# Kernel tuning notes

Hardware: AMD Instinct MI355X
Metric: run time of the kernel (lower is better)

Reference implementation:

```python
import jax, jax.numpy as jnp
import numpy as np
from jax import lax

# ---- Loihi neuron constants (params['neuron'], params['simulation']) ----
VTH_MANT = 80
THETA = VTH_MANT * (1 << 6)          # 5120, vThMant scaled by 2^6 weight resolution
I_DECAY = 1024                        # current decay (12-bit fixed point)
V_DECAY = 128                         # voltage decay (12-bit fixed point)
WGT_EXP = 0
WGT_SCALE = 1 << (6 + WGT_EXP)        # 64
TS = 1.0

def _loihi_srm_kernel():
    # integer Loihi simulation of the PSP impulse response (slayerLoihi._calculateLoihiPSP)
    u = 1 << (6 + WGT_EXP)
    v = u
    ker = [v]
    while ker[-1] > 0:
        u = (u * (4096 - I_DECAY)) >> 12
        v = ((v * (4096 - V_DECAY)) >> 12) + u
        ker.append(v)
    return np.asarray(ker, np.float32) / (1 << 6)

SRM_KERNEL = _loihi_srm_kernel()      # ~180 taps, ker[0] = 1

def psp(x):
    # causal FIR over time: y[t] = sum_k x[t-k] * ker[k];  x: [B, C, T]
    B, C, T = x.shape
    K = SRM_KERNEL.shape[0]
    w = jnp.asarray(SRM_KERNEL[::-1].copy()).reshape(1, 1, K).astype(x.dtype)
    y = lax.conv_general_dilated(x.reshape(B * C, 1, T), w, (1,), [(K - 1, 0)],
                                 dimension_numbers=('NCH', 'OIH', 'NCH'))
    return y.reshape(B, C, T)

def _decay(x, d):
    # sign-symmetric arithmetic-shift decay, exactly as the Loihi CUDA kernel
    s = jnp.where(x >= 0, 1, -1).astype(jnp.int32)
    return s * ((s * x * (4096 - d)) >> 12)

def spike_loihi(w):
    # quantized integrate-and-fire; w: [B, C, T] float weighted input
    x = jnp.trunc(w * (WGT_SCALE / TS)).astype(jnp.int32)   # C-style int() truncation
    xt = jnp.moveaxis(x, -1, 0)                             # [T, B, C]
    z = jnp.zeros(x.shape[:-1], jnp.int32)
    def step(carry, xi):
        u, v = carry
        un = _decay(u, I_DECAY) + xi
        vn = _decay(v, V_DECAY) + un
        sp = vn >= THETA
        vn = jnp.where(sp, 0, vn)                           # hard reset on spike
        return (un, vn), (sp, vn)
    _, (s, vrec) = lax.scan(step, (z, z), xt)
    spike = jnp.moveaxis(s, 0, -1).astype(w.dtype) / TS
    voltage = jnp.moveaxis(vrec, 0, -1).astype(w.dtype)
    return spike, voltage

def delay_shift(x):
    # delayShift(x, 1): one-tick axonal delay along time
    return jnp.concatenate([jnp.zeros_like(x[..., :1]), x[..., :-1]], axis=-1)

def setup_inputs():
    key = jax.random.key(0)
    k1, k2, k3 = jax.random.split(key, 3)
    B, CIN, HID, COUT, T = 32, 512, 1024, 256, 512
    spike_input = (jax.random.uniform(k1, (B, CIN, 1, 1, T)) < 0.05).astype(jnp.float32)
    W1 = jax.random.normal(k2, (HID, CIN), jnp.float32) * 0.2
    W2 = jax.random.normal(k3, (COUT, HID), jnp.float32) * 0.2
    return {"spike_input": spike_input, "W1": W1, "W2": W2}

def reference(spike_input, W1, W2):
    x = spike_input[:, :, 0, 0, :]                          # [B, Cin, T]
    s1, _ = spike_loihi(psp(jnp.einsum('oi,bit->bot', W1, x)))
    s1 = delay_shift(s1)
    s2, _ = spike_loihi(psp(jnp.einsum('oh,bht->bot', W2, s1)))
    s2 = delay_shift(s2)
    return s2[:, :, None, None, :]                          # [B, Cout, 1, 1, T]
```

## Files before the change

### kernel.cpp

```cpp
#include <hip/hip_runtime.h>


#pragma clang fp contract(off)

constexpr int kT     = 512;
constexpr int kCIN   = 512;
constexpr int kHID   = 1024;
constexpr int kCOUT  = 256;
constexpr int kB     = 32;
constexpr int kTHETA = 5120;
constexpr int kOT1   = 16;
constexpr int kOT2   = 8;
constexpr int kHP1   = 20;
constexpr int kHP2   = 12;
constexpr int kSBP   = 516;
constexpr int kCURP  = 521;

struct Ker { float v[96]; int n; };
constexpr Ker mk_ker() {
    Ker K{}; int u = 64, v = 64; K.v[0] = 1.0f; int i = 1;
    while (v > 0 && i < 96) {
        u = (u * 3072) >> 12;
        v = ((v * 3968) >> 12) + u;
        K.v[i++] = (float)v / 64.0f;
    }
    K.n = i; return K;
}
constexpr Ker KER = mk_ker();
static_assert(KER.n == 88, "SRM kernel length must be 88");
static_assert(KER.v[87] == 0.0f, "tap 87 must be the exact zero tail tap");
__device__ __constant__ Ker KERC = mk_ker();

__device__ __forceinline__ float2 pkmul(const float2 a, const float b) {
    return make_float2(a.x * b, a.y * b);
}
__device__ __forceinline__ float2 pkadd(const float2 a, const float2 b) {
    return make_float2(a.x + b.x, a.y + b.y);
}

__device__ __forceinline__ int decay_i(int x, int mult) {
    unsigned ax = (x >= 0) ? (unsigned)x : (0u - (unsigned)x);
    unsigned p  = ax * (unsigned)mult;
    int sh = ((int)p) >> 12;
    return (x >= 0) ? sh : (int)(0u - (unsigned)sh);
}

__global__ __launch_bounds__(256) void k0_pack(const float* __restrict__ X,
                                               unsigned* __restrict__ XPW) {
    const int tid = blockIdx.x * 256 + threadIdx.x;
    const int b = tid >> 13, rem = tid & 8191, w = rem >> 9, t = rem & 511;
    const float* xp = X + ((size_t)(b * kCIN + w * 32)) * kT + t;
    unsigned m = 0;
#pragma unroll
    for (int k = 0; k < 32; ++k)
        m |= (xp[(size_t)k * kT] != 0.0f ? 1u : 0u) << k;
    XPW[tid] = m;
}

#define GW16(MW, BASE) { unsigned m_ = (MW); while (m_) { \
    const int bi_ = __ffs(m_) - 1; m_ &= m_ - 1; const int ii_ = (BASE) + bi_; \
    const float4 f0 = *reinterpret_cast<const float4*>(&w0[ii_ * 4]); \
    const float4 f1 = *reinterpret_cast<const float4*>(&w1[ii_ * 4]); \
    const float4 f2 = *reinterpret_cast<const float4*>(&w2[ii_ * 4]); \
    const float4 f3 = *reinterpret_cast<const float4*>(&w3[ii_ * 4]); \
    A0 = pkadd(A0, make_float2(f0.x, f0.y)); A1 = pkadd(A1, make_float2(f0.z, f0.w)); \
    A2 = pkadd(A2, make_float2(f1.x, f1.y)); A3 = pkadd(A3, make_float2(f1.z, f1.w)); \
    A4 = pkadd(A4, make_float2(f2.x, f2.y)); A5 = pkadd(A5, make_float2(f2.z, f2.w)); \
    A6 = pkadd(A6, make_float2(f3.x, f3.y)); A7 = pkadd(A7, make_float2(f3.z, f3.w)); } }

#define ACC16(E0,E1,E2,E3,E4,E5,E6,E7, Q0,Q1,Q2,Q3, KV) \
    E0 = pkadd(E0, pkmul(make_float2(Q0.x, Q0.y), (KV))); \
    E1 = pkadd(E1, pkmul(make_float2(Q0.z, Q0.w), (KV))); \
    E2 = pkadd(E2, pkmul(make_float2(Q1.x, Q1.y), (KV))); \
    E3 = pkadd(E3, pkmul(make_float2(Q1.z, Q1.w), (KV))); \
    E4 = pkadd(E4, pkmul(make_float2(Q2.x, Q2.y), (KV))); \
    E5 = pkadd(E5, pkmul(make_float2(Q2.z, Q2.w), (KV))); \
    E6 = pkadd(E6, pkmul(make_float2(Q3.x, Q3.y), (KV))); \
    E7 = pkadd(E7, pkmul(make_float2(Q3.z, Q3.w), (KV)));

__global__ __launch_bounds__(512, 6) void k1_fused(const unsigned* __restrict__ XPW,
                                                   const float* __restrict__ W,
                                                   unsigned short* __restrict__ SPW) {
    __shared__ __align__(16) unsigned char regn[40960];
    __shared__ unsigned char sbuf[kOT1 * kSBP];

    float* w0    = reinterpret_cast<float*>(regn);
    float* w1    = reinterpret_cast<float*>(regn + 8192);
    float* w2    = reinterpret_cast<float*>(regn + 16384);
    float* w3    = reinterpret_cast<float*>(regn + 24576);
    float* heven = reinterpret_cast<float*>(regn);
    float* hodd  = reinterpret_cast<float*>(regn + 20480);
    int*   cur   = reinterpret_cast<int*>(regn);

    const int t     = threadIdx.x;
    const int b     = blockIdx.x >> 6;
    const int oblk  = blockIdx.x & 63;
    const int obase = oblk * kOT1;

    for (int idx = t; idx < kOT1 * kCIN; idx += 512) {
        const int j = idx >> 9, i = idx & 511;
        float* wq = reinterpret_cast<float*>(regn + (j >> 2) * 8192);
        wq[i * 4 + (j & 3)] = W[(size_t)(obase + j) * kCIN + i];
    }
    __syncthreads();

    const unsigned* xw = XPW + ((size_t)b * 16) * kT + t;
    float2 A0 = make_float2(0.f, 0.f), A1 = A0, A2 = A0, A3 = A0,
           A4 = A0, A5 = A0, A6 = A0, A7 = A0;
    {
        const unsigned m0=xw[0],    m1=xw[512],  m2=xw[1024], m3=xw[1536],
                       m4=xw[2048], m5=xw[2560], m6=xw[3072], m7=xw[3584],
                       m8=xw[4096], m9=xw[4608], mA=xw[5120], mB=xw[5632],
                       mC=xw[6144], mD=xw[6656], mE=xw[7168], mF=xw[7680];
        GW16(m0,0)   GW16(m1,32)  GW16(m2,64)  GW16(m3,96)
        GW16(m4,128) GW16(m5,160) GW16(m6,192) GW16(m7,224)
        GW16(m8,256) GW16(m9,288) GW16(mA,320) GW16(mB,352)
        GW16(mC,384) GW16(mD,416) GW16(mE,448) GW16(mF,480)
    }
    __syncthreads();

    {
        float* hr = ((t & 1) ? hodd : heven) + (size_t)(t >> 1) * kHP1;
        *reinterpret_cast<float4*>(hr + 0)  = make_float4(A0.x, A0.y, A1.x, A1.y);
        *reinterpret_cast<float4*>(hr + 4)  = make_float4(A2.x, A2.y, A3.x, A3.y);
        *reinterpret_cast<float4*>(hr + 8)  = make_float4(A4.x, A4.y, A5.x, A5.y);
        *reinterpret_cast<float4*>(hr + 12) = make_float4(A6.x, A6.y, A7.x, A7.y);
    }
    __syncthreads();

    float2 E0, E1, E2, E3, E4, E5, E6, E7, O0, O1, O2, O3, O4, O5, O6, O7;
    E0=E1=E2=E3=E4=E5=E6=E7=O0=O1=O2=O3=O4=O5=O6=O7 = make_float2(0.f, 0.f);
    const int q = t;
    if (t < 256) {
        for (int j = 0; j < 43; ++j) {
            const int m = q - 43 + j;
            const float t87 = KERC.v[87 - 2 * j];
            const float t86 = KERC.v[86 - 2 * j];
            const float t85 = KERC.v[85 - 2 * j];
            if (m >= 0) {
                const float* he = heven + (size_t)m * kHP1;
                const float* ho = hodd  + (size_t)m * kHP1;
                const float4 a0 = *reinterpret_cast<const float4*>(he + 0);
                const float4 a1 = *reinterpret_cast<const float4*>(he + 4);
                const float4 a2 = *reinterpret_cast<const float4*>(he + 8);
                const float4 a3 = *reinterpret_cast<const float4*>(he + 12);
                const float4 b0 = *reinterpret_cast<const float4*>(ho + 0);
                const float4 b1 = *reinterpret_cast<const float4*>(ho + 4);
                const float4 b2 = *reinterpret_cast<const float4*>(ho + 8);
                const float4 b3 = *reinterpret_cast<const float4*>(ho + 12);
                ACC16(E0,E1,E2,E3,E4,E5,E6,E7, a0,a1,a2,a3, t86)
                ACC16(E0,E1,E2,E3,E4,E5,E6,E7, b0,b1,b2,b3, t85)
                ACC16(O0,O1,O2,O3,O4,O5,O6,O7, a0,a1,a2,a3, t87)
                ACC16(O0,O1,O2,O3,O4,O5,O6,O7, b0,b1,b2,b3, t86)
            }
        }
        {
            const float* he = heven + (size_t)q * kHP1;
            const float* ho = hodd  + (size_t)q * kHP1;
            const float4 a0 = *reinterpret_cast<const float4*>(he + 0);
            const float4 a1 = *reinterpret_cast<const float4*>(he + 4);
            const float4 a2 = *reinterpret_cast<const float4*>(he + 8);
            const float4 a3 = *reinterpret_cast<const float4*>(he + 12);
            const float4 b0 = *reinterpret_cast<const float4*>(ho + 0);
            const float4 b1 = *reinterpret_cast<const float4*>(ho + 4);
            const float4 b2 = *reinterpret_cast<const float4*>(ho + 8);
            const float4 b3 = *reinterpret_cast<const float4*>(ho + 12);
            const float v1 = KERC.v[1];
            ACC16(E0,E1,E2,E3,E4,E5,E6,E7, a0,a1,a2,a3, 1.0f)
            ACC16(O0,O1,O2,O3,O4,O5,O6,O7, a0,a1,a2,a3, v1)
            ACC16(O0,O1,O2,O3,O4,O5,O6,O7, b0,b1,b2,b3, 1.0f)
        }
    }
    __syncthreads();

    if (t < 256) {
#define CST1(CH, EV, OV) \
        cur[(CH) * kCURP + 2 * q]     = (int)((EV) * 64.0f); \
        cur[(CH) * kCURP + 2 * q + 1] = (int)((OV) * 64.0f);
        CST1( 0, E0.x, O0.x) CST1( 1, E0.y, O0.y)
        CST1( 2, E1.x, O1.x) CST1( 3, E1.y, O1.y)
        CST1( 4, E2.x, O2.x) CST1( 5, E2.y, O2.y)
        CST1( 6, E3.x, O3.x) CST1( 7, E3.y, O3.y)
        CST1( 8, E4.x, O4.x) CST1( 9, E4.y, O4.y)
        CST1(10, E5.x, O5.x) CST1(11, E5.y, O5.y)
        CST1(12, E6.x, O6.x) CST1(13, E6.y, O6.y)
        CST1(14, E7.x, O7.x) CST1(15, E7.y, O7.y)
#undef CST1
    }
    __syncthreads();

    if (t < kOT1) {
        const int* cr = cur + t * kCURP;
        int u = 0, v = 0;
        sbuf[t * kSBP + 0] = 0;
        for (int s = 0; s < kT; ++s) {
            const int un = (int)((unsigned)decay_i(u, 3072) + (unsigned)cr[s]);
            int vn = (int)((unsigned)decay_i(v, 3968) + (unsigned)un);
            const int sp_ = (vn >= kTHETA) ? 1 : 0;
            if (sp_) vn = 0;
            u = un; v = vn;
            if (s + 1 < kT) sbuf[t * kSBP + s + 1] = (unsigned char)sp_;
        }
    }
    __syncthreads();

    {
        unsigned lo = 0, hi = 0;
#pragma unroll
        for (int j = 0; j < 8; ++j) {
            lo |= (unsigned)sbuf[j * kSBP + t] << j;
            hi |= (unsigned)sbuf[(8 + j) * kSBP + t] << j;
        }
        SPW[((((size_t)b * 32 + (oblk >> 1)) * kT) + t) * 2 + (oblk & 1)] =
            (unsigned short)(lo | (hi << 8));
    }
}

#define GW8(MW, BASE) { unsigned m_ = (MW); while (m_) { \
    const int bi_ = __ffs(m_) - 1; m_ &= m_ - 1; const int ii_ = (BASE) + bi_; \
    const float4 lo = *reinterpret_cast<const float4*>(&wlo[ii_ * 4]); \
    const float4 hi = *reinterpret_cast<const float4*>(&whi[ii_ * 4]); \
    A0 = pkadd(A0, make_float2(lo.x, lo.y)); A1 = pkadd(A1, make_float2(lo.z, lo.w)); \
    A2 = pkadd(A2, make_float2(hi.x, hi.y)); A3 = pkadd(A3, make_float2(hi.z, hi.w)); } }

#define ACC8(E0,E1,E2,E3, Q0,Q1, KV) \
    E0 = pkadd(E0, pkmul(make_float2(Q0.x, Q0.y), (KV))); \
    E1 = pkadd(E1, pkmul(make_float2(Q0.z, Q0.w), (KV))); \
    E2 = pkadd(E2, pkmul(make_float2(Q1.x, Q1.y), (KV))); \
    E3 = pkadd(E3, pkmul(make_float2(Q1.z, Q1.w), (KV)));

__global__ __launch_bounds__(512, 8) void k2_fused(const unsigned* __restrict__ SPW,
                                                   const float* __restrict__ W,
                                                   float* __restrict__ O) {
    __shared__ __align__(16) unsigned char regn[32768];
    __shared__ unsigned char sbuf[kOT2 * kSBP];

    float* wlo   = reinterpret_cast<float*>(regn);
    float* whi   = reinterpret_cast<float*>(regn + 16384);
    float* heven = reinterpret_cast<float*>(regn);
    float* hodd  = reinterpret_cast<float*>(regn + 12288);
    int*   cur   = reinterpret_cast<int*>(regn);

    const int t     = threadIdx.x;
    const int b     = blockIdx.x >> 5;
    const int obase = (blockIdx.x & 31) * kOT2;

    for (int idx = t; idx < kOT2 * kHID; idx += 512) {
        const int j = idx >> 10, i = idx & 1023;
        const float w = W[(size_t)(obase + j) * kHID + i];
        if (j < 4) wlo[i * 4 + j] = w; else whi[i * 4 + (j - 4)] = w;
    }
    __syncthreads();

    const unsigned* sp = SPW + ((size_t)b * 32) * kT + t;
    float2 A0 = make_float2(0.f, 0.f), A1 = A0, A2 = A0, A3 = A0;
#pragma unroll 4
    for (int g = 0; g < 32; ++g) {
        const unsigned m = sp[(size_t)g * kT];
        GW8(m, g * 32)
    }
    __syncthreads();

    {
        float* hr = ((t & 1) ? hodd : heven) + (size_t)(t >> 1) * kHP2;
        *reinterpret_cast<float4*>(hr + 0) = make_float4(A0.x, A0.y, A1.x, A1.y);
        *reinterpret_cast<float4*>(hr + 4) = make_float4(A2.x, A2.y, A3.x, A3.y);
    }
    __syncthreads();

    float2 E0, E1, E2, E3, O0, O1, O2, O3;
    E0=E1=E2=E3=O0=O1=O2=O3 = make_float2(0.f, 0.f);
    const int q = t;
    if (t < 256) {
        for (int j = 0; j < 43; ++j) {
            const int m = q - 43 + j;
            const float t87 = KERC.v[87 - 2 * j];
            const float t86 = KERC.v[86 - 2 * j];
            const float t85 = KERC.v[85 - 2 * j];
            if (m >= 0) {
                const float* he = heven + (size_t)m * kHP2;
                const float* ho = hodd  + (size_t)m * kHP2;
                const float4 a0 = *reinterpret_cast<const float4*>(he + 0);
                const float4 a1 = *reinterpret_cast<const float4*>(he + 4);
                const float4 b0 = *reinterpret_cast<const float4*>(ho + 0);
                const float4 b1 = *reinterpret_cast<const float4*>(ho + 4);
                ACC8(E0,E1,E2,E3, a0,a1, t86)
                ACC8(E0,E1,E2,E3, b0,b1, t85)
                ACC8(O0,O1,O2,O3, a0,a1, t87)
                ACC8(O0,O1,O2,O3, b0,b1, t86)
            }
        }
        {
            const float* he = heven + (size_t)q * kHP2;
            const float* ho = hodd  + (size_t)q * kHP2;
            const float4 a0 = *reinterpret_cast<const float4*>(he + 0);
            const float4 a1 = *reinterpret_cast<const float4*>(he + 4);
            const float4 b0 = *reinterpret_cast<const float4*>(ho + 0);
            const float4 b1 = *reinterpret_cast<const float4*>(ho + 4);
            const float v1 = KERC.v[1];
            ACC8(E0,E1,E2,E3, a0,a1, 1.0f)
            ACC8(O0,O1,O2,O3, a0,a1, v1)
            ACC8(O0,O1,O2,O3, b0,b1, 1.0f)
        }
    }
    __syncthreads();

    if (t < 256) {
#define CST2(CH, EV, OV) \
        cur[(CH) * kCURP + 2 * q]     = (int)((EV) * 64.0f); \
        cur[(CH) * kCURP + 2 * q + 1] = (int)((OV) * 64.0f);
        CST2(0, E0.x, O0.x) CST2(1, E0.y, O0.y)
        CST2(2, E1.x, O1.x) CST2(3, E1.y, O1.y)
        CST2(4, E2.x, O2.x) CST2(5, E2.y, O2.y)
        CST2(6, E3.x, O3.x) CST2(7, E3.y, O3.y)
#undef CST2
    }
    __syncthreads();

    if (t < kOT2) {
        const int* cr = cur + t * kCURP;
        int u = 0, v = 0;
        sbuf[t * kSBP + 0] = 0;
        for (int s = 0; s < kT; ++s) {
            const int un = (int)((unsigned)decay_i(u, 3072) + (unsigned)cr[s]);
            int vn = (int)((unsigned)decay_i(v, 3968) + (unsigned)un);
            const int sp2 = (vn >= kTHETA) ? 1 : 0;
            if (sp2) vn = 0;
            u = un; v = vn;
            if (s + 1 < kT) sbuf[t * kSBP + s + 1] = (unsigned char)sp2;
        }
    }
    __syncthreads();

    for (int idx = t; idx < kOT2 * kT; idx += 512) {
        const int j = idx >> 9, tt = idx & 511;
        O[((size_t)(b * kCOUT + obase + j)) * kT + tt] = (float)sbuf[j * kSBP + tt];
    }
}

__global__ void k_mark(float* __restrict__ out0, float v) {
    if (threadIdx.x == 0 && blockIdx.x == 0) out0[0] = v;
}

extern "C" void kernel_launch(void* const* d_in, const int* in_sizes, int n_in,
                              void* d_out, int out_size, void* d_ws, size_t ws_size,
                              hipStream_t stream) {
    const float* X  = (const float*)d_in[0];
    const float* W1 = (const float*)d_in[1];
    const float* W2 = (const float*)d_in[2];
    float* OUT = (float*)d_out;

    const size_t xpw_bytes = (size_t)kB * 16 * kT * 4;
    const size_t spw_bytes = (size_t)kB * 32 * kT * 4;
    const size_t need = xpw_bytes + spw_bytes;

    if (n_in != 3 || in_sizes[0] != kB * kCIN * kT || in_sizes[1] != kHID * kCIN ||
        in_sizes[2] != kCOUT * kHID || out_size != kB * kCOUT * kT) {
        hipLaunchKernelGGL(k_mark, dim3(1), dim3(64), 0, stream, OUT, 7000001.0f);
        return;
    }
    if (ws_size < need || d_ws == nullptr) {
        const float v = (float)(8000000u + (unsigned)((ws_size >> 10) % 900000));
        hipLaunchKernelGGL(k_mark, dim3(1), dim3(64), 0, stream, OUT, v);
        return;
    }

    unsigned*       xpw = (unsigned*)d_ws;
    unsigned short* spw = (unsigned short*)((char*)d_ws + xpw_bytes);

    hipLaunchKernelGGL(k0_pack, dim3(kB * 16 * kT / 256), dim3(256), 0, stream,
                       X, xpw);
    hipLaunchKernelGGL(k1_fused, dim3(kB * (kHID / kOT1)), dim3(512), 0, stream,
                       xpw, W1, spw);
    hipLaunchKernelGGL(k2_fused, dim3(kB * (kCOUT / kOT2)), dim3(512), 0, stream,
                       (const unsigned*)spw, W2, OUT);
}
```

Baseline: 395.9 us.

## Precompute per-timestep spike index lists for layer-1 gather; vectorize current stores

Adds a kernel that converts the packed input bitmasks into compact per-(batch,time) lists of active input indices, capped at 128 entries. Layer 1 then walks these lists eight entries at a time instead of scanning 16 bitmask words with ffs loops in each of its 64 blocks per batch. The current stores now use int2 writes, and the LIF scan reads two steps per load. The cap truncates silently if more than 128 inputs fire at one step, which is very unlikely at 5% density. The change also adds an extra launch and workspace traffic.

```diff
diff --git a/kernel.cpp b/kernel.cpp
--- a/kernel.cpp
+++ b/kernel.cpp
@@ -14,7 +14,8 @@
 constexpr int kHP1   = 20;
 constexpr int kHP2   = 12;
 constexpr int kSBP   = 516;
-constexpr int kCURP  = 521;
+constexpr int kCURP  = 522;
+constexpr int kLCAP  = 128;
 
 struct Ker { float v[96]; int n; };
 constexpr Ker mk_ker() {
@@ -57,8 +58,26 @@
     XPW[tid] = m;
 }
 
-#define GW16(MW, BASE) { unsigned m_ = (MW); while (m_) { \
-    const int bi_ = __ffs(m_) - 1; m_ &= m_ - 1; const int ii_ = (BASE) + bi_; \
+__global__ __launch_bounds__(256) void k0b_list(const unsigned* __restrict__ XPW,
+                                                unsigned short* __restrict__ XL,
+                                                unsigned short* __restrict__ XC) {
+    const int bt = blockIdx.x * 256 + threadIdx.x;
+    const int b = bt >> 9, t = bt & 511;
+    const unsigned* xw = XPW + ((size_t)b * 16) * kT + t;
+    unsigned short* row = XL + (size_t)bt * kLCAP;
+    int cnt = 0;
+    for (int w = 0; w < 16; ++w) {
+        unsigned m = xw[(size_t)w * kT];
+        while (m) {
+            const int bi = __ffs(m) - 1; m &= m - 1;
+            if (cnt < kLCAP) row[cnt] = (unsigned short)(w * 32 + bi);
+            ++cnt;
+        }
+    }
+    XC[bt] = (unsigned short)min(cnt, kLCAP);
+}
+
+#define GADD16(II) { const int ii_ = (II); \
     const float4 f0 = *reinterpret_cast<const float4*>(&w0[ii_ * 4]); \
     const float4 f1 = *reinterpret_cast<const float4*>(&w1[ii_ * 4]); \
     const float4 f2 = *reinterpret_cast<const float4*>(&w2[ii_ * 4]); \
@@ -66,7 +85,7 @@
     A0 = pkadd(A0, make_float2(f0.x, f0.y)); A1 = pkadd(A1, make_float2(f0.z, f0.w)); \
     A2 = pkadd(A2, make_float2(f1.x, f1.y)); A3 = pkadd(A3, make_float2(f1.z, f1.w)); \
     A4 = pkadd(A4, make_float2(f2.x, f2.y)); A5 = pkadd(A5, make_float2(f2.z, f2.w)); \
-    A6 = pkadd(A6, make_float2(f3.x, f3.y)); A7 = pkadd(A7, make_float2(f3.z, f3.w)); } }
+    A6 = pkadd(A6, make_float2(f3.x, f3.y)); A7 = pkadd(A7, make_float2(f3.z, f3.w)); }
 
 #define ACC16(E0,E1,E2,E3,E4,E5,E6,E7, Q0,Q1,Q2,Q3, KV) \
     E0 = pkadd(E0, pkmul(make_float2(Q0.x, Q0.y), (KV))); \
@@ -78,7 +97,8 @@
     E6 = pkadd(E6, pkmul(make_float2(Q3.x, Q3.y), (KV))); \
     E7 = pkadd(E7, pkmul(make_float2(Q3.z, Q3.w), (KV)));
 
-__global__ __launch_bounds__(512, 6) void k1_fused(const unsigned* __restrict__ XPW,
+__global__ __launch_bounds__(512, 6) void k1_fused(const unsigned short* __restrict__ XL,
+                                                   const unsigned short* __restrict__ XC,
                                                    const float* __restrict__ W,
                                                    unsigned short* __restrict__ SPW) {
     __shared__ __align__(16) unsigned char regn[40960];
@@ -104,18 +124,20 @@
     }
     __syncthreads();
 
-    const unsigned* xw = XPW + ((size_t)b * 16) * kT + t;
+    const int bt = (b << 9) | t;
+    const int cnt = XC[bt];
+    const uint4* lrow = reinterpret_cast<const uint4*>(XL + (size_t)bt * kLCAP);
     float2 A0 = make_float2(0.f, 0.f), A1 = A0, A2 = A0, A3 = A0,
            A4 = A0, A5 = A0, A6 = A0, A7 = A0;
-    {
-        const unsigned m0=xw[0],    m1=xw[512],  m2=xw[1024], m3=xw[1536],
-                       m4=xw[2048], m5=xw[2560], m6=xw[3072], m7=xw[3584],
-                       m8=xw[4096], m9=xw[4608], mA=xw[5120], mB=xw[5632],
-                       mC=xw[6144], mD=xw[6656], mE=xw[7168], mF=xw[7680];
-        GW16(m0,0)   GW16(m1,32)  GW16(m2,64)  GW16(m3,96)
-        GW16(m4,128) GW16(m5,160) GW16(m6,192) GW16(m7,224)
-        GW16(m8,256) GW16(m9,288) GW16(mA,320) GW16(mB,352)
-        GW16(mC,384) GW16(mD,416) GW16(mE,448) GW16(mF,480)
+    for (int k8 = 0; k8 * 8 < cnt; ++k8) {
+        const uint4 le = lrow[k8];
+        const int base = k8 * 8;
+#define GE1(E, V) if (base + (E) < cnt) GADD16((int)(V))
+        GE1(0, le.x & 0xffffu) GE1(1, le.x >> 16)
+        GE1(2, le.y & 0xffffu) GE1(3, le.y >> 16)
+        GE1(4, le.z & 0xffffu) GE1(5, le.z >> 16)
+        GE1(6, le.w & 0xffffu) GE1(7, le.w >> 16)
+#undef GE1
     }
     __syncthreads();
 
@@ -175,8 +197,8 @@
 
     if (t < 256) {
 #define CST1(CH, EV, OV) \
-        cur[(CH) * kCURP + 2 * q]     = (int)((EV) * 64.0f); \
-        cur[(CH) * kCURP + 2 * q + 1] = (int)((OV) * 64.0f);
+        *reinterpret_cast<int2*>(cur + (CH) * kCURP + 2 * q) = \
+            make_int2((int)((EV) * 64.0f), (int)((OV) * 64.0f));
         CST1( 0, E0.x, O0.x) CST1( 1, E0.y, O0.y)
         CST1( 2, E1.x, O1.x) CST1( 3, E1.y, O1.y)
         CST1( 4, E2.x, O2.x) CST1( 5, E2.y, O2.y)
@@ -190,16 +212,27 @@
     __syncthreads();
 
     if (t < kOT1) {
-        const int* cr = cur + t * kCURP;
+        const int2* cr2 = reinterpret_cast<const int2*>(cur + t * kCURP);
         int u = 0, v = 0;
         sbuf[t * kSBP + 0] = 0;
-        for (int s = 0; s < kT; ++s) {
-            const int un = (int)((unsigned)decay_i(u, 3072) + (unsigned)cr[s]);
-            int vn = (int)((unsigned)decay_i(v, 3968) + (unsigned)un);
-            const int sp_ = (vn >= kTHETA) ? 1 : 0;
-            if (sp_) vn = 0;
-            u = un; v = vn;
-            if (s + 1 < kT) sbuf[t * kSBP + s + 1] = (unsigned char)sp_;
+        for (int s2 = 0; s2 < 256; ++s2) {
+            const int2 c2 = cr2[s2];
+            {
+                const int un = (int)((unsigned)decay_i(u, 3072) + (unsigned)c2.x);
+                int vn = (int)((unsigned)decay_i(v, 3968) + (unsigned)un);
+                const int sp_ = (vn >= kTHETA) ? 1 : 0;
+                if (sp_) vn = 0;
+                u = un; v = vn;
+                sbuf[t * kSBP + 2 * s2 + 1] = (unsigned char)sp_;
+            }
+            {
+                const int un = (int)((unsigned)decay_i(u, 3072) + (unsigned)c2.y);
+                int vn = (int)((unsigned)decay_i(v, 3968) + (unsigned)un);
+                const int sp_ = (vn >= kTHETA) ? 1 : 0;
+                if (sp_) vn = 0;
+                u = un; v = vn;
+                if (2 * s2 + 2 < kT) sbuf[t * kSBP + 2 * s2 + 2] = (unsigned char)sp_;
+            }
         }
     }
     __syncthreads();
@@ -307,8 +340,8 @@
 
     if (t < 256) {
 #define CST2(CH, EV, OV) \
-        cur[(CH) * kCURP + 2 * q]     = (int)((EV) * 64.0f); \
-        cur[(CH) * kCURP + 2 * q + 1] = (int)((OV) * 64.0f);
+        *reinterpret_cast<int2*>(cur + (CH) * kCURP + 2 * q) = \
+            make_int2((int)((EV) * 64.0f), (int)((OV) * 64.0f));
         CST2(0, E0.x, O0.x) CST2(1, E0.y, O0.y)
         CST2(2, E1.x, O1.x) CST2(3, E1.y, O1.y)
         CST2(4, E2.x, O2.x) CST2(5, E2.y, O2.y)
@@ -318,16 +351,27 @@
     __syncthreads();
 
     if (t < kOT2) {
-        const int* cr = cur + t * kCURP;
+        const int2* cr2 = reinterpret_cast<const int2*>(cur + t * kCURP);
         int u = 0, v = 0;
         sbuf[t * kSBP + 0] = 0;
-        for (int s = 0; s < kT; ++s) {
-            const int un = (int)((unsigned)decay_i(u, 3072) + (unsigned)cr[s]);
-            int vn = (int)((unsigned)decay_i(v, 3968) + (unsigned)un);
-            const int sp2 = (vn >= kTHETA) ? 1 : 0;
-            if (sp2) vn = 0;
-            u = un; v = vn;
-            if (s + 1 < kT) sbuf[t * kSBP + s + 1] = (unsigned char)sp2;
+        for (int s2 = 0; s2 < 256; ++s2) {
+            const int2 c2 = cr2[s2];
+            {
+                const int un = (int)((unsigned)decay_i(u, 3072) + (unsigned)c2.x);
+                int vn = (int)((unsigned)decay_i(v, 3968) + (unsigned)un);
+                const int sp2 = (vn >= kTHETA) ? 1 : 0;
+                if (sp2) vn = 0;
+                u = un; v = vn;
+                sbuf[t * kSBP + 2 * s2 + 1] = (unsigned char)sp2;
+            }
+            {
+                const int un = (int)((unsigned)decay_i(u, 3072) + (unsigned)c2.y);
+                int vn = (int)((unsigned)decay_i(v, 3968) + (unsigned)un);
+                const int sp2 = (vn >= kTHETA) ? 1 : 0;
+                if (sp2) vn = 0;
+                u = un; v = vn;
+                if (2 * s2 + 2 < kT) sbuf[t * kSBP + 2 * s2 + 2] = (unsigned char)sp2;
+            }
         }
     }
     __syncthreads();
@@ -352,7 +396,9 @@
 
     const size_t xpw_bytes = (size_t)kB * 16 * kT * 4;
     const size_t spw_bytes = (size_t)kB * 32 * kT * 4;
-    const size_t need = xpw_bytes + spw_bytes;
+    const size_t xl_bytes  = (size_t)kB * kT * kLCAP * 2;
+    const size_t xc_bytes  = (size_t)kB * kT * 2;
+    const size_t need = xpw_bytes + spw_bytes + xl_bytes + xc_bytes;
 
     if (n_in != 3 || in_sizes[0] != kB * kCIN * kT || in_sizes[1] != kHID * kCIN ||
         in_sizes[2] != kCOUT * kHID || out_size != kB * kCOUT * kT) {
@@ -365,13 +411,18 @@
         return;
     }
 
-    unsigned*       xpw = (unsigned*)d_ws;
-    unsigned short* spw = (unsigned short*)((char*)d_ws + xpw_bytes);
+    char* ws = (char*)d_ws;
+    unsigned*       xpw = (unsigned*)ws;
+    unsigned short* spw = (unsigned short*)(ws + xpw_bytes);
+    unsigned short* xl  = (unsigned short*)(ws + xpw_bytes + spw_bytes);
+    unsigned short* xc  = (unsigned short*)(ws + xpw_bytes + spw_bytes + xl_bytes);
 
     hipLaunchKernelGGL(k0_pack, dim3(kB * 16 * kT / 256), dim3(256), 0, stream,
                        X, xpw);
+    hipLaunchKernelGGL(k0b_list, dim3(kB * kT / 256), dim3(256), 0, stream,
+                       xpw, xl, xc);
     hipLaunchKernelGGL(k1_fused, dim3(kB * (kHID / kOT1)), dim3(512), 0, stream,
-                       xpw, W1, spw);
+                       xl, xc, W1, spw);
     hipLaunchKernelGGL(k2_fused, dim3(kB * (kCOUT / kOT2)), dim3(512), 0, stream,
                        (const unsigned*)spw, W2, OUT);
 }
```

New measurement: 390.5 us. Within noise of the previous version (-1.4%).
